# Optimization experiments

Hardware: AMD Instinct MI355X
Metric: run time of the kernel (lower is better)

Reference implementation:

```python
import jax, jax.numpy as jnp
import numpy as np

TEMPERATURE = 0.5
HEAD_DIM = 64
NUM_HEADS = 4

N_NODES = 50000
N_EDGES = 800000
DIM = 256


def setup_inputs() -> dict:
    key = jax.random.key(0)
    ks = jax.random.split(key, 7)
    h = jax.random.normal(ks[0], (N_NODES, DIM), dtype=jnp.float32)
    src = jax.random.randint(ks[1], (N_EDGES,), 0, N_NODES)
    dst = jax.random.randint(ks[2], (N_EDGES,), 0, N_NODES)
    attn_q = jax.random.normal(ks[3], (DIM, NUM_HEADS * HEAD_DIM), dtype=jnp.float32) * 0.02
    attn_k = jax.random.normal(ks[4], (DIM, NUM_HEADS * HEAD_DIM), dtype=jnp.float32) * 0.02
    W = jax.random.normal(ks[5], (DIM, DIM), dtype=jnp.float32) * (1.0 / np.sqrt(DIM))
    b = jnp.zeros((DIM,), dtype=jnp.float32)
    return {"h": h, "src": src, "dst": dst, "attn_q": attn_q, "attn_k": attn_k, "W": W, "b": b}


def _edge_softmax_by_dst(a, dst, n_nodes):
    # softmax over incoming edges of each destination node (DGL edge_softmax)
    m = jax.ops.segment_max(a, dst, num_segments=n_nodes)
    e = jnp.exp(a - m[dst])
    s = jax.ops.segment_sum(e, dst, num_segments=n_nodes)
    return e / s[dst]


def reference(h, src, dst, attn_q, attn_k, W, b):
    n = h.shape[0]
    v = h @ W.T + b                         # iv Linear: [N, D]
    q = h @ attn_q                          # [N, H*64]
    k = h @ attn_k                          # [N, H*64]
    # per-edge score: mean over heads then over head_dim == mean over all H*64,
    # preceded by /8 -> dot(q_src, k_dst) / (8 * H * 64)
    scale = 1.0 / (8.0 * NUM_HEADS * HEAD_DIM)
    a = jnp.einsum('ed,ed->e', q[src], k[dst]) * scale   # [E]
    # global standardization over all edges (std unbiased=False)
    m = a.mean()
    s = jnp.sqrt(((a - m) ** 2).mean())
    a = (a - m) / s / TEMPERATURE
    a = _edge_softmax_by_dst(a, dst, n)     # [E]
    # message passing: sum_{e: dst(e)=i} a_e * v[src(e)]
    out = jax.ops.segment_sum(v[src] * a[:, None], dst, num_segments=n)  # [N, D]
    return out, a
```

## Files before the change

kernel.cpp:

```cpp
#include <hip/hip_runtime.h>
#include <math.h>

#define DIM 256
#define NQKV 768
#define STAT_BLOCKS 2048

typedef float  f32x4 __attribute__((ext_vector_type(4)));
typedef short  bs8   __attribute__((ext_vector_type(8)));

__device__ __forceinline__ ushort f2bf(float f) {
    unsigned int u = __float_as_uint(f);
    u += 0x7fffu + ((u >> 16) & 1u);
    return (ushort)(u >> 16);
}
__device__ __forceinline__ float bf2f(ushort u) {
    return __uint_as_float(((unsigned int)u) << 16);
}
__device__ __forceinline__ float dotu4(uint4 a, uint4 b) {
    float s;
    s  = bf2f((ushort)a.x) * bf2f((ushort)b.x) + bf2f((ushort)(a.x >> 16)) * bf2f((ushort)(b.x >> 16));
    s += bf2f((ushort)a.y) * bf2f((ushort)b.y) + bf2f((ushort)(a.y >> 16)) * bf2f((ushort)(b.y >> 16));
    s += bf2f((ushort)a.z) * bf2f((ushort)b.z) + bf2f((ushort)(a.z >> 16)) * bf2f((ushort)(b.z >> 16));
    s += bf2f((ushort)a.w) * bf2f((ushort)b.w) + bf2f((ushort)(a.w >> 16)) * bf2f((ushort)(b.w >> 16));
    return s;
}

#define MFMA16(c, a, b) \
    asm("s_nop 1\n\tv_mfma_f32_16x16x32_bf16 %0, %1, %2, %0" : "+v"(c) : "v"(a), "v"(b))

__global__ __launch_bounds__(256) void conv_h(
    const float* __restrict__ h, ushort* __restrict__ h_bf, int total8)
{
    const int idx = blockIdx.x * 256 + threadIdx.x;
    if (idx >= total8) return;
    const float4* hp = (const float4*)(h + (size_t)idx * 8);
    float4 a = hp[0], b = hp[1];
    uint4 o;
    o.x = (unsigned)f2bf(a.x) | ((unsigned)f2bf(a.y) << 16);
    o.y = (unsigned)f2bf(a.z) | ((unsigned)f2bf(a.w) << 16);
    o.z = (unsigned)f2bf(b.x) | ((unsigned)f2bf(b.y) << 16);
    o.w = (unsigned)f2bf(b.z) | ((unsigned)f2bf(b.w) << 16);
    *(uint4*)(h_bf + (size_t)idx * 8) = o;
}

__global__ __launch_bounds__(256) void build_bt(
    const float* __restrict__ attn_q, const float* __restrict__ attn_k,
    const float* __restrict__ W, ushort* __restrict__ bt)
{
    const int n = blockIdx.x;
    const int k = threadIdx.x;
    float val;
    if (n < 256)      val = attn_q[(size_t)k * 256 + n];
    else if (n < 512) val = attn_k[(size_t)k * 256 + (n - 256)];
    else              val = W[(size_t)(n - 512) * 256 + k];
    bt[(size_t)n * 256 + k] = f2bf(val);
}

__global__ __launch_bounds__(256) void gemm_qkv_mfma(
    const ushort* __restrict__ h_bf, const ushort* __restrict__ bt,
    const float* __restrict__ bias, ushort* __restrict__ qkv, int M)
{
    __shared__ __align__(16) ushort As[128 * 40];
    __shared__ __align__(16) ushort Bs[128 * 40];

    const int bm = blockIdx.x * 128;
    const int bn = blockIdx.y * 128;
    const int t    = threadIdx.x;
    const int lane = t & 63;
    const int wid  = t >> 6;
    const int wm   = wid >> 1;
    const int wn   = wid & 1;
    const int fr   = lane & 15;
    const int ko   = (lane >> 4) * 8;

    f32x4 acc[4][4];
    #pragma unroll
    for (int i = 0; i < 4; ++i)
        #pragma unroll
        for (int j = 0; j < 4; ++j)
            acc[i][j] = (f32x4){0.f, 0.f, 0.f, 0.f};

    for (int k0 = 0; k0 < DIM; k0 += 32) {
        #pragma unroll
        for (int ii = 0; ii < 2; ++ii) {
            const int s   = t * 2 + ii;
            const int row = s >> 2;
            const int sl  = s & 3;
            int ga = bm + row; if (ga > M - 1) ga = M - 1;
            uint4 va = *(const uint4*)(h_bf + (size_t)ga * 256 + k0 + sl * 8);
            *(uint4*)(As + row * 40 + sl * 8) = va;
            uint4 vb = *(const uint4*)(bt + (size_t)(bn + row) * 256 + k0 + sl * 8);
            *(uint4*)(Bs + row * 40 + sl * 8) = vb;
        }
        __syncthreads();

        bs8 af[4], bf_[4];
        #pragma unroll
        for (int f = 0; f < 4; ++f) {
            af[f]  = *(const bs8*)(As + (wm * 64 + f * 16 + fr) * 40 + ko);
            bf_[f] = *(const bs8*)(Bs + (wn * 64 + f * 16 + fr) * 40 + ko);
        }
        #pragma unroll
        for (int fm = 0; fm < 4; ++fm)
            #pragma unroll
            for (int fn = 0; fn < 4; ++fn)
                MFMA16(acc[fm][fn], af[fm], bf_[fn]);

        __syncthreads();
    }

    asm volatile("s_nop 7\n\ts_nop 7\n\ts_nop 7" ::: );

    #pragma unroll
    for (int fm = 0; fm < 4; ++fm) {
        const int rowbase = bm + wm * 64 + fm * 16 + (lane >> 4) * 4;
        #pragma unroll
        for (int fn = 0; fn < 4; ++fn) {
            const int col = bn + wn * 64 + fn * 16 + fr;
            float bv = (col >= 512) ? bias[col - 512] : 0.f;
            #pragma unroll
            for (int r = 0; r < 4; ++r) {
                const int row = rowbase + r;
                if (row < M)
                    qkv[(size_t)row * NQKV + col] = f2bf(acc[fm][fn][r] + bv);
            }
        }
    }
}

__global__ __launch_bounds__(256) void deg_count(
    const int* __restrict__ dst, int* __restrict__ deg, int E)
{
    const int e = blockIdx.x * 256 + threadIdx.x;
    if (e < E) atomicAdd(&deg[dst[e]], 1);
}

__global__ __launch_bounds__(1024) void scan_rowptr(
    const int* __restrict__ deg, int* __restrict__ row_ptr, int N)
{
    const int tid  = threadIdx.x;
    const int lane = tid & 63;
    const int wv   = tid >> 6;

    if (tid == 0) row_ptr[0] = 0;

    __shared__ int woff[17];
    __shared__ int carryS;
    if (tid == 0) carryS = 0;
    __syncthreads();

    for (int base = 0; base < N; base += 4096) {
        int x[4], pre[4];
        int run = 0;
        #pragma unroll
        for (int j = 0; j < 4; ++j) {
            const int i = base + tid * 4 + j;
            const int v = (i < N) ? deg[i] : 0;
            pre[j] = run; x[j] = v; run += v;
        }
        int incl = run;
        #pragma unroll
        for (int off = 1; off < 64; off <<= 1) {
            int y = __shfl_up(incl, off);
            if (lane >= off) incl += y;
        }
        const int wex = incl - run;
        if (lane == 63) woff[wv] = incl;
        __syncthreads();
        if (wv == 0) {
            int wtot = (lane < 16) ? woff[lane] : 0;
            int winc = wtot;
            #pragma unroll
            for (int off = 1; off < 16; off <<= 1) {
                int y = __shfl_up(winc, off);
                if (lane >= off) winc += y;
            }
            if (lane < 16) woff[lane] = winc - wtot;
            if (lane == 15) woff[16] = winc;
        }
        __syncthreads();
        const int basev = carryS + woff[wv] + wex;
        #pragma unroll
        for (int j = 0; j < 4; ++j) {
            const int i = base + tid * 4 + j;
            if (i < N) row_ptr[i + 1] = basev + pre[j] + x[j];
        }
        __syncthreads();
        if (tid == 0) carryS += woff[16];
        __syncthreads();
    }
}

__global__ __launch_bounds__(256) void scatter_edges(
    const int* __restrict__ src, const int* __restrict__ dst,
    const int* __restrict__ row_ptr, int* __restrict__ cursor,
    int4* __restrict__ edata, int E)
{
    const int e = blockIdx.x * 256 + threadIdx.x;
    if (e < E) {
        const int d = dst[e];
        const int pos = row_ptr[d] + atomicAdd(&cursor[d], 1);
        edata[pos] = make_int4(src[e], d, e, 0);
    }
}

__global__ __launch_bounds__(256) void edge_dot_csr(
    const ushort* __restrict__ qkv, const int4* __restrict__ edata,
    float* __restrict__ a_rawc, double* __restrict__ partials, int E)
{
    const int lane = threadIdx.x & 63;
    const int wid  = threadIdx.x >> 6;
    const int lq   = lane & 31;
    const int hh   = lane >> 5;
    const int w    = blockIdx.x * 4 + wid;
    const int nw   = gridDim.x * 4;
    const int chunk = (E + nw - 1) / nw;
    const int p0 = min(E, w * chunk);
    const int p1 = min(E, p0 + chunk);

    double lsum = 0.0, lsum2 = 0.0;
    int p = p0;

    for (; p + 8 <= p1; p += 8) {
        const int4 ed0 = edata[p     + hh];
        const int4 ed1 = edata[p + 2 + hh];
        const int4 ed2 = edata[p + 4 + hh];
        const int4 ed3 = edata[p + 6 + hh];
        uint4 q0 = *(const uint4*)(qkv + (size_t)ed0.x * NQKV + lq * 8);
        uint4 q1 = *(const uint4*)(qkv + (size_t)ed1.x * NQKV + lq * 8);
        uint4 q2 = *(const uint4*)(qkv + (size_t)ed2.x * NQKV + lq * 8);
        uint4 q3 = *(const uint4*)(qkv + (size_t)ed3.x * NQKV + lq * 8);
        uint4 k0 = *(const uint4*)(qkv + (size_t)ed0.y * NQKV + 256 + lq * 8);
        uint4 k1 = *(const uint4*)(qkv + (size_t)ed1.y * NQKV + 256 + lq * 8);
        uint4 k2 = *(const uint4*)(qkv + (size_t)ed2.y * NQKV + 256 + lq * 8);
        uint4 k3 = *(const uint4*)(qkv + (size_t)ed3.y * NQKV + 256 + lq * 8);
        float d0 = dotu4(q0, k0);
        float d1 = dotu4(q1, k1);
        float d2 = dotu4(q2, k2);
        float d3 = dotu4(q3, k3);
        #pragma unroll
        for (int off = 16; off; off >>= 1) {
            d0 += __shfl_xor(d0, off);
            d1 += __shfl_xor(d1, off);
            d2 += __shfl_xor(d2, off);
            d3 += __shfl_xor(d3, off);
        }
        if (lq == 0) {
            a_rawc[p     + hh] = d0;
            a_rawc[p + 2 + hh] = d1;
            a_rawc[p + 4 + hh] = d2;
            a_rawc[p + 6 + hh] = d3;
            lsum  += (double)d0 + (double)d1 + (double)d2 + (double)d3;
            lsum2 += (double)d0 * d0 + (double)d1 * d1
                   + (double)d2 * d2 + (double)d3 * d3;
        }
    }
    for (; p + 2 <= p1; p += 2) {
        const int4 ed0 = edata[p + hh];
        uint4 q0 = *(const uint4*)(qkv + (size_t)ed0.x * NQKV + lq * 8);
        uint4 k0 = *(const uint4*)(qkv + (size_t)ed0.y * NQKV + 256 + lq * 8);
        float d0 = dotu4(q0, k0);
        #pragma unroll
        for (int off = 16; off; off >>= 1) d0 += __shfl_xor(d0, off);
        if (lq == 0) {
            a_rawc[p + hh] = d0;
            lsum  += (double)d0;
            lsum2 += (double)d0 * d0;
        }
    }
    if (p < p1) {
        const int4 ed0 = edata[p];
        uint4 q0 = *(const uint4*)(qkv + (size_t)ed0.x * NQKV + lq * 8);
        uint4 k0 = *(const uint4*)(qkv + (size_t)ed0.y * NQKV + 256 + lq * 8);
        float d0 = dotu4(q0, k0);
        #pragma unroll
        for (int off = 16; off; off >>= 1) d0 += __shfl_xor(d0, off);
        if (lane == 0) {
            a_rawc[p] = d0;
            lsum  += (double)d0;
            lsum2 += (double)d0 * d0;
        }
    }

    lsum  += __shfl_xor(lsum, 32);
    lsum2 += __shfl_xor(lsum2, 32);

    __shared__ double bsum[4], bsum2[4];
    if (lane == 0) { bsum[wid] = lsum; bsum2[wid] = lsum2; }
    __syncthreads();
    if (threadIdx.x == 0) {
        partials[blockIdx.x]             = bsum[0] + bsum[1] + bsum[2] + bsum[3];
        partials[gridDim.x + blockIdx.x] = bsum2[0] + bsum2[1] + bsum2[2] + bsum2[3];
    }
}

__global__ __launch_bounds__(256) void finalize_coef(
    const double* __restrict__ partials, float* __restrict__ coef, int E)
{
    __shared__ double red[256];
    const int tid = threadIdx.x;
    double s1 = 0.0, s2 = 0.0;
    for (int i = tid; i < STAT_BLOCKS; i += 256) {
        s1 += partials[i];
        s2 += partials[STAT_BLOCKS + i];
    }
    red[tid] = s1;
    __syncthreads();
    for (int off = 128; off; off >>= 1) {
        if (tid < off) red[tid] += red[tid + off];
        __syncthreads();
    }
    const double tot1 = red[0];
    __syncthreads();
    red[tid] = s2;
    __syncthreads();
    for (int off = 128; off; off >>= 1) {
        if (tid < off) red[tid] += red[tid + off];
        __syncthreads();
    }
    if (tid == 0) {
        const double mean = tot1 / (double)E;
        const double var  = red[0] / (double)E - mean * mean;
        coef[0] = (float)mean;
        coef[1] = (float)(1.0 / (sqrt(var) * 0.5));
    }
}

__global__ __launch_bounds__(256) void agg_fused(
    const ushort* __restrict__ qkv, const float* __restrict__ a_rawc,
    const int4* __restrict__ edata, const int* __restrict__ row_ptr,
    const float* __restrict__ coef,
    float* __restrict__ out, float* __restrict__ a_out, int N)
{
    const int node = blockIdx.x;
    const int tid  = threadIdx.x;
    const int lane = tid & 63;
    const int wv   = tid >> 6;
    const int s  = row_ptr[node];
    const int en = row_ptr[node + 1];
    const float mean = coef[0];
    const float mul  = coef[1];

    float lsum = 0.f;
    for (int j = s + tid; j < en; j += 256)
        lsum += __expf((a_rawc[j] - mean) * mul);
    #pragma unroll
    for (int off = 32; off; off >>= 1) lsum += __shfl_xor(lsum, off);
    __shared__ float ws4[4];
    if (lane == 0) ws4[wv] = lsum;
    __syncthreads();
    const float rcp = 1.0f / (ws4[0] + ws4[1] + ws4[2] + ws4[3]);

    float4 acc = make_float4(0.f, 0.f, 0.f, 0.f);
    int j = s + wv;
    for (; j + 4 < en; j += 8) {
        const int4 edA = edata[j];
        const int4 edB = edata[j + 4];
        const float wA = __expf((a_rawc[j]     - mean) * mul) * rcp;
        const float wB = __expf((a_rawc[j + 4] - mean) * mul) * rcp;
        ushort4 vA = *(const ushort4*)(qkv + (size_t)edA.x * NQKV + 512 + lane * 4);
        ushort4 vB = *(const ushort4*)(qkv + (size_t)edB.x * NQKV + 512 + lane * 4);
        if (lane == 0) { a_out[edA.z] = wA; a_out[edB.z] = wB; }
        acc.x += wA * bf2f(vA.x) + wB * bf2f(vB.x);
        acc.y += wA * bf2f(vA.y) + wB * bf2f(vB.y);
        acc.z += wA * bf2f(vA.z) + wB * bf2f(vB.z);
        acc.w += wA * bf2f(vA.w) + wB * bf2f(vB.w);
    }
    if (j < en) {
        const int4 edA = edata[j];
        const float wA = __expf((a_rawc[j] - mean) * mul) * rcp;
        ushort4 vA = *(const ushort4*)(qkv + (size_t)edA.x * NQKV + 512 + lane * 4);
        if (lane == 0) a_out[edA.z] = wA;
        acc.x += wA * bf2f(vA.x);
        acc.y += wA * bf2f(vA.y);
        acc.z += wA * bf2f(vA.z);
        acc.w += wA * bf2f(vA.w);
    }

    __shared__ float lds[4][DIM];
    *(float4*)&lds[wv][lane * 4] = acc;
    __syncthreads();
    out[(size_t)node * DIM + tid] =
        lds[0][tid] + lds[1][tid] + lds[2][tid] + lds[3][tid];
}

extern "C" void kernel_launch(void* const* d_in, const int* in_sizes, int n_in,
                              void* d_out, int out_size, void* d_ws, size_t ws_size,
                              hipStream_t stream)
{
    const float* h      = (const float*)d_in[0];
    const int*   src    = (const int*)d_in[1];
    const int*   dst    = (const int*)d_in[2];
    const float* attn_q = (const float*)d_in[3];
    const float* attn_k = (const float*)d_in[4];
    const float* W      = (const float*)d_in[5];
    const float* bias   = (const float*)d_in[6];

    const int N = in_sizes[0] / DIM;
    const int E = in_sizes[1];

    float* out   = (float*)d_out;
    float* a_out = out + (size_t)N * DIM;

    char* ws = (char*)d_ws;
    ushort* h_bf  = (ushort*)ws;
    int4*   edata = (int4*)ws;
    ws += (size_t)N * DIM * 2;
    ushort* qkv   = (ushort*)ws; ws += (size_t)N * NQKV * 2;
    ushort* bt    = (ushort*)ws; ws += (size_t)NQKV * DIM * 2;
    float* a_rawc = (float*)ws;  ws += (size_t)E * 4;
    int* deg      = (int*)ws;    ws += (size_t)N * 4;
    int* cursor   = (int*)ws;    ws += (size_t)N * 4;
    double* partials = (double*)ws; ws += (size_t)STAT_BLOCKS * 2 * 8;
    float* coef   = (float*)ws;  ws += 8;
    int* row_ptr  = (int*)ws;    ws += (size_t)(N + 1) * 4;

    hipMemsetAsync(deg,    0, (size_t)N * 4, stream);
    hipMemsetAsync(cursor, 0, (size_t)N * 4, stream);

    const int total8 = N * DIM / 8;
    conv_h<<<(total8 + 255) / 256, 256, 0, stream>>>(h, h_bf, total8);
    build_bt<<<NQKV, 256, 0, stream>>>(attn_q, attn_k, W, bt);

    dim3 gg((N + 127) / 128, NQKV / 128);
    gemm_qkv_mfma<<<gg, 256, 0, stream>>>(h_bf, bt, bias, qkv, N);

    deg_count<<<(E + 255) / 256, 256, 0, stream>>>(dst, deg, E);
    scan_rowptr<<<1, 1024, 0, stream>>>(deg, row_ptr, N);
    scatter_edges<<<(E + 255) / 256, 256, 0, stream>>>(src, dst, row_ptr, cursor, edata, E);
    edge_dot_csr<<<STAT_BLOCKS, 256, 0, stream>>>(qkv, edata, a_rawc, partials, E);
    finalize_coef<<<1, 256, 0, stream>>>(partials, coef, E);
    agg_fused<<<N, 256, 0, stream>>>(qkv, a_rawc, edata, row_ptr, coef, out, a_out, N);
}
```

Measured before the change: 461.9 us.

## Use direct global-to-LDS loads in QKV GEMM and one wave per node in aggregation

The GEMM tile load now uses global_load_lds with an XOR-swizzled, unpadded LDS layout instead of register-staged copies, which cuts VGPR traffic and LDS store instructions. The aggregation kernel now gives each node a single wavefront, four nodes per block, instead of a whole block. Edge weights and source indices are staged in per-wave LDS buffers so four gathered value rows can be in flight at once, and the block-level reduction and syncs are gone. The price is less parallelism for very high-degree nodes and a full vmcnt wait before each GEMM barrier.

```diff
diff --git a/kernel.cpp b/kernel.cpp
--- a/kernel.cpp
+++ b/kernel.cpp
@@ -27,6 +27,10 @@
 
 #define MFMA16(c, a, b) \
     asm("s_nop 1\n\tv_mfma_f32_16x16x32_bf16 %0, %1, %2, %0" : "+v"(c) : "v"(a), "v"(b))
+
+#define GLOAD_LDS16(g, l) __builtin_amdgcn_global_load_lds( \
+    (const __attribute__((address_space(1))) unsigned int*)(g), \
+    (__attribute__((address_space(3))) unsigned int*)(l), 16, 0, 0)
 
 __global__ __launch_bounds__(256) void conv_h(
     const float* __restrict__ h, ushort* __restrict__ h_bf, int total8)
@@ -60,8 +64,8 @@
     const ushort* __restrict__ h_bf, const ushort* __restrict__ bt,
     const float* __restrict__ bias, ushort* __restrict__ qkv, int M)
 {
-    __shared__ __align__(16) ushort As[128 * 40];
-    __shared__ __align__(16) ushort Bs[128 * 40];
+    __shared__ __align__(16) ushort As[128 * 32];
+    __shared__ __align__(16) ushort Bs[128 * 32];
 
     const int bm = blockIdx.x * 128;
     const int bn = blockIdx.y * 128;
@@ -71,7 +75,14 @@
     const int wm   = wid >> 1;
     const int wn   = wid & 1;
     const int fr   = lane & 15;
-    const int ko   = (lane >> 4) * 8;
+
+    const int srow0 = wid * 32 + (lane >> 2);
+    const int srow1 = srow0 + 16;
+    const int g0 = (lane & 3) ^ (srow0 & 3);
+    const int g1 = (lane & 3) ^ (srow1 & 3);
+    const int ga0 = min(bm + srow0, M - 1);
+    const int ga1 = min(bm + srow1, M - 1);
+    const int rchunk = ((lane >> 4) ^ (fr & 3)) * 8;
 
     f32x4 acc[4][4];
     #pragma unroll
@@ -81,24 +92,18 @@
             acc[i][j] = (f32x4){0.f, 0.f, 0.f, 0.f};
 
     for (int k0 = 0; k0 < DIM; k0 += 32) {
-        #pragma unroll
-        for (int ii = 0; ii < 2; ++ii) {
-            const int s   = t * 2 + ii;
-            const int row = s >> 2;
-            const int sl  = s & 3;
-            int ga = bm + row; if (ga > M - 1) ga = M - 1;
-            uint4 va = *(const uint4*)(h_bf + (size_t)ga * 256 + k0 + sl * 8);
-            *(uint4*)(As + row * 40 + sl * 8) = va;
-            uint4 vb = *(const uint4*)(bt + (size_t)(bn + row) * 256 + k0 + sl * 8);
-            *(uint4*)(Bs + row * 40 + sl * 8) = vb;
-        }
+        GLOAD_LDS16(h_bf + (size_t)ga0 * 256 + k0 + g0 * 8, As + (wid * 32) * 32);
+        GLOAD_LDS16(h_bf + (size_t)ga1 * 256 + k0 + g1 * 8, As + (wid * 32 + 16) * 32);
+        GLOAD_LDS16(bt + (size_t)(bn + srow0) * 256 + k0 + g0 * 8, Bs + (wid * 32) * 32);
+        GLOAD_LDS16(bt + (size_t)(bn + srow1) * 256 + k0 + g1 * 8, Bs + (wid * 32 + 16) * 32);
+        asm volatile("s_waitcnt vmcnt(0)" ::: "memory");
         __syncthreads();
 
         bs8 af[4], bf_[4];
         #pragma unroll
         for (int f = 0; f < 4; ++f) {
-            af[f]  = *(const bs8*)(As + (wm * 64 + f * 16 + fr) * 40 + ko);
-            bf_[f] = *(const bs8*)(Bs + (wn * 64 + f * 16 + fr) * 40 + ko);
+            af[f]  = *(const bs8*)(As + (wm * 64 + f * 16 + fr) * 32 + rchunk);
+            bf_[f] = *(const bs8*)(Bs + (wn * 64 + f * 16 + fr) * 32 + rchunk);
         }
         #pragma unroll
         for (int fm = 0; fm < 4; ++fm)
@@ -332,56 +337,68 @@
     const float* __restrict__ coef,
     float* __restrict__ out, float* __restrict__ a_out, int N)
 {
-    const int node = blockIdx.x;
-    const int tid  = threadIdx.x;
-    const int lane = tid & 63;
-    const int wv   = tid >> 6;
-    const int s  = row_ptr[node];
-    const int en = row_ptr[node + 1];
+    const int lane = threadIdx.x & 63;
+    const int wv   = threadIdx.x >> 6;
+    const int node = blockIdx.x * 4 + wv;
+    if (node >= N) return;
+
+    const int s   = row_ptr[node];
+    const int deg = row_ptr[node + 1] - s;
     const float mean = coef[0];
     const float mul  = coef[1];
 
+    __shared__ float wbuf_s[4][128];
+    __shared__ int   sbuf_s[4][128];
+    float* wbuf = wbuf_s[wv];
+    int*   sbuf = sbuf_s[wv];
+
     float lsum = 0.f;
-    for (int j = s + tid; j < en; j += 256)
-        lsum += __expf((a_rawc[j] - mean) * mul);
+    for (int j = lane; j < deg; j += 64)
+        lsum += __expf((a_rawc[s + j] - mean) * mul);
     #pragma unroll
     for (int off = 32; off; off >>= 1) lsum += __shfl_xor(lsum, off);
-    __shared__ float ws4[4];
-    if (lane == 0) ws4[wv] = lsum;
-    __syncthreads();
-    const float rcp = 1.0f / (ws4[0] + ws4[1] + ws4[2] + ws4[3]);
+    const float rcp = 1.0f / lsum;
 
     float4 acc = make_float4(0.f, 0.f, 0.f, 0.f);
-    int j = s + wv;
-    for (; j + 4 < en; j += 8) {
-        const int4 edA = edata[j];
-        const int4 edB = edata[j + 4];
-        const float wA = __expf((a_rawc[j]     - mean) * mul) * rcp;
-        const float wB = __expf((a_rawc[j + 4] - mean) * mul) * rcp;
-        ushort4 vA = *(const ushort4*)(qkv + (size_t)edA.x * NQKV + 512 + lane * 4);
-        ushort4 vB = *(const ushort4*)(qkv + (size_t)edB.x * NQKV + 512 + lane * 4);
-        if (lane == 0) { a_out[edA.z] = wA; a_out[edB.z] = wB; }
-        acc.x += wA * bf2f(vA.x) + wB * bf2f(vB.x);
-        acc.y += wA * bf2f(vA.y) + wB * bf2f(vB.y);
-        acc.z += wA * bf2f(vA.z) + wB * bf2f(vB.z);
-        acc.w += wA * bf2f(vA.w) + wB * bf2f(vB.w);
-    }
-    if (j < en) {
-        const int4 edA = edata[j];
-        const float wA = __expf((a_rawc[j] - mean) * mul) * rcp;
-        ushort4 vA = *(const ushort4*)(qkv + (size_t)edA.x * NQKV + 512 + lane * 4);
-        if (lane == 0) a_out[edA.z] = wA;
-        acc.x += wA * bf2f(vA.x);
-        acc.y += wA * bf2f(vA.y);
-        acc.z += wA * bf2f(vA.z);
-        acc.w += wA * bf2f(vA.w);
-    }
-
-    __shared__ float lds[4][DIM];
-    *(float4*)&lds[wv][lane * 4] = acc;
-    __syncthreads();
-    out[(size_t)node * DIM + tid] =
-        lds[0][tid] + lds[1][tid] + lds[2][tid] + lds[3][tid];
+    for (int b0 = 0; b0 < deg; b0 += 128) {
+        const int bc = min(128, deg - b0);
+        for (int j = lane; j < bc; j += 64) {
+            const int4 ed = edata[s + b0 + j];
+            const float wgt = __expf((a_rawc[s + b0 + j] - mean) * mul) * rcp;
+            wbuf[j] = wgt;
+            sbuf[j] = ed.x;
+            a_out[ed.z] = wgt;
+        }
+        asm volatile("s_waitcnt lgkmcnt(0)" ::: "memory");
+        __builtin_amdgcn_sched_barrier(0);
+
+        int j = 0;
+        for (; j + 4 <= bc; j += 4) {
+            const float w0 = wbuf[j],     w1 = wbuf[j + 1];
+            const float w2 = wbuf[j + 2], w3 = wbuf[j + 3];
+            const int   s0 = sbuf[j],     s1 = sbuf[j + 1];
+            const int   s2 = sbuf[j + 2], s3 = sbuf[j + 3];
+            ushort4 v0 = *(const ushort4*)(qkv + (size_t)s0 * NQKV + 512 + lane * 4);
+            ushort4 v1 = *(const ushort4*)(qkv + (size_t)s1 * NQKV + 512 + lane * 4);
+            ushort4 v2 = *(const ushort4*)(qkv + (size_t)s2 * NQKV + 512 + lane * 4);
+            ushort4 v3 = *(const ushort4*)(qkv + (size_t)s3 * NQKV + 512 + lane * 4);
+            acc.x += w0 * bf2f(v0.x) + w1 * bf2f(v1.x) + w2 * bf2f(v2.x) + w3 * bf2f(v3.x);
+            acc.y += w0 * bf2f(v0.y) + w1 * bf2f(v1.y) + w2 * bf2f(v2.y) + w3 * bf2f(v3.y);
+            acc.z += w0 * bf2f(v0.z) + w1 * bf2f(v1.z) + w2 * bf2f(v2.z) + w3 * bf2f(v3.z);
+            acc.w += w0 * bf2f(v0.w) + w1 * bf2f(v1.w) + w2 * bf2f(v2.w) + w3 * bf2f(v3.w);
+        }
+        for (; j < bc; ++j) {
+            const float w0 = wbuf[j];
+            const int   s0 = sbuf[j];
+            ushort4 v0 = *(const ushort4*)(qkv + (size_t)s0 * NQKV + 512 + lane * 4);
+            acc.x += w0 * bf2f(v0.x);
+            acc.y += w0 * bf2f(v0.y);
+            acc.z += w0 * bf2f(v0.z);
+            acc.w += w0 * bf2f(v0.w);
+        }
+    }
+
+    *(float4*)&out[(size_t)node * DIM + lane * 4] = acc;
 }
 
 extern "C" void kernel_launch(void* const* d_in, const int* in_sizes, int n_in,
@@ -430,5 +447,5 @@
     scatter_edges<<<(E + 255) / 256, 256, 0, stream>>>(src, dst, row_ptr, cursor, edata, E);
     edge_dot_csr<<<STAT_BLOCKS, 256, 0, stream>>>(qkv, edata, a_rawc, partials, E);
     finalize_coef<<<1, 256, 0, stream>>>(partials, coef, E);
-    agg_fused<<<N, 256, 0, stream>>>(qkv, a_rawc, edata, row_ptr, coef, out, a_out, N);
-}
+    agg_fused<<<(N + 3) / 4, 256, 0, stream>>>(qkv, a_rawc, edata, row_ptr, coef, out, a_out, N);
+}
```

Result: faster. 422.3 us (-8.6%).
